# Kernel optimization log

Hardware: AMD Instinct MI355X
Metric: run time of the kernel (lower is better)

## Reference

```python
import jax, jax.numpy as jnp
import numpy as np

EMBED = 1024
B, T = 4, 2048

def setup_inputs() -> dict:
    key = jax.random.key(0)
    k1, k2, k3, k4, k5 = jax.random.split(key, 5)
    s_in = 1.0 / np.sqrt(EMBED)
    return {
        "x": jax.random.normal(k1, (B, T, EMBED), dtype=jnp.float32),
        "w_qkv": jax.random.normal(k2, (3 * EMBED, EMBED), dtype=jnp.float32) * s_in,  # torch Linear layout [out,in]
        "b_qkv": jax.random.normal(k3, (3 * EMBED,), dtype=jnp.float32) * 0.01,
        "w_proj": jax.random.normal(k4, (EMBED, EMBED), dtype=jnp.float32) * s_in,
        "b_proj": jax.random.normal(k5, (EMBED,), dtype=jnp.float32) * 0.01,
    }

def reference(x, w_qkv, b_qkv, w_proj, b_proj):
    Bq, Tq, C = x.shape
    qkv = jnp.einsum('btc,oc->bto', x, w_qkv) + b_qkv        # [B,T,3C]
    q, k, v = jnp.split(qkv, 3, axis=-1)                      # each [B,T,C]
    att = jnp.einsum('btc,bsc->bts', q, k) / jnp.sqrt(jnp.float32(C))  # [B,T,T]
    causal = jnp.tril(jnp.ones((Tq, Tq), dtype=bool))
    att = jnp.where(causal[None, :, :], att, -jnp.inf)
    att = jax.nn.softmax(att, axis=-1)
    out = jnp.einsum('bts,bsc->btc', att, v)                   # [B,T,C]
    return jnp.einsum('btc,oc->bto', out, w_proj) + b_proj
```

## Files before the change

kernel.cpp:

```cpp
#include <hip/hip_runtime.h>
#include <hip/hip_bf16.h>

typedef __hip_bfloat16 bf16;
typedef __attribute__((ext_vector_type(8))) short bf16x8;
typedef __attribute__((ext_vector_type(4))) float f32x4;

#define GLD16(gp, lp) __builtin_amdgcn_global_load_lds( \
    (const __attribute__((address_space(1))) void*)(gp), \
    (__attribute__((address_space(3))) void*)(lp), 16, 0, 0)

__global__ __launch_bounds__(256) void cvt_bf16(const float* __restrict__ in,
                                                bf16* __restrict__ out) {
    int i = (blockIdx.x * 256 + threadIdx.x) * 4;
    float4 f = *(const float4*)&in[i];
    __hip_bfloat162 p0, p1;
    p0.x = __float2bfloat16(f.x); p0.y = __float2bfloat16(f.y);
    p1.x = __float2bfloat16(f.z); p1.y = __float2bfloat16(f.w);
    *(__hip_bfloat162*)&out[i]     = p0;
    *(__hip_bfloat162*)&out[i + 2] = p1;
}

__global__ __launch_bounds__(256) void cvt_weights(
    const float* __restrict__ wq, bf16* __restrict__ wqo,
    const float* __restrict__ wp, bf16* __restrict__ wpo) {
    int blk = blockIdx.x;
    const float* in; bf16* out; int base;
    if (blk < 3072) { in = wq; out = wqo; base = blk; }
    else            { in = wp; out = wpo; base = blk - 3072; }
    int i = (base * 256 + threadIdx.x) * 4;
    float4 f = *(const float4*)&in[i];
    __hip_bfloat162 p0, p1;
    p0.x = __float2bfloat16(f.x); p0.y = __float2bfloat16(f.y);
    p1.x = __float2bfloat16(f.z); p1.y = __float2bfloat16(f.w);
    *(__hip_bfloat162*)&out[i]     = p0;
    *(__hip_bfloat162*)&out[i + 2] = p1;
}

__global__ void transpose_v(const bf16* __restrict__ V, bf16* __restrict__ Vt) {
    __shared__ bf16 tile[32][33];
    const int b = blockIdx.z;
    const int c0 = blockIdx.x * 32, t0 = blockIdx.y * 32;
    const int tx = threadIdx.x, ty = threadIdx.y;
    #pragma unroll
    for (int i = 0; i < 32; i += 8)
        tile[ty + i][tx] = V[((size_t)(b * 2048 + t0 + ty + i)) * 1024 + c0 + tx];
    __syncthreads();
    #pragma unroll
    for (int i = 0; i < 32; i += 8)
        Vt[((size_t)b * 1024 + c0 + ty + i) * 2048 + t0 + tx] = tile[tx][ty + i];
}

__global__ __launch_bounds__(256) void rowsum_p(const bf16* __restrict__ P,
                                                float* __restrict__ rs) {
    const int row = blockIdx.x;
    const int t = row & 2047;
    const int ncol = ((t >> 8) + 1) << 8;
    const bf16* prow = P + (size_t)row * 2048;
    const int tid = threadIdx.x;
    float s = 0.f;
    if (tid * 8 < ncol) {
        bf16x8 v = *(const bf16x8*)&prow[tid * 8];
        #pragma unroll
        for (int i = 0; i < 8; ++i)
            s += __bfloat162float(((const bf16*)&v)[i]);
    }
    #pragma unroll
    for (int off = 32; off; off >>= 1) s += __shfl_xor(s, off);
    __shared__ float red[4];
    const int wave = tid >> 6, lane = tid & 63;
    if (lane == 0) red[wave] = s;
    __syncthreads();
    if (tid == 0) rs[row] = red[0] + red[1] + red[2] + red[3];
}

template<int MODE>
__global__ __launch_bounds__(512, 2) void gemm256(
    const bf16* __restrict__ A, const bf16* __restrict__ B,
    const float* __restrict__ bias,
    void* __restrict__ out0, void* __restrict__ out1, void* __restrict__ out2)
{
    __shared__ bf16 As[2][256][64];
    __shared__ bf16 Bs[2][256][64];
    constexpr int LDA = (MODE == 2) ? 2048 : 1024;
    constexpr int LDB = (MODE == 2) ? 2048 : 1024;

    const int nwgx = gridDim.x;
    const int nwg = nwgx * gridDim.y;
    int wg = blockIdx.y * nwgx + blockIdx.x;
    wg = (wg & 7) * (nwg >> 3) + (wg >> 3);
    const int bx = wg % nwgx, by = wg / nwgx, bz = blockIdx.z;

    if (MODE == 1 && bx > by) return;
    const int NT = (MODE == 2) ? 4 * (by + 1) : 16;
    const int m0 = by * 256, n0 = bx * 256;

    const bf16* Ab = A;
    const bf16* Bb = B;
    if (MODE == 1) { Ab += (size_t)bz * (2048ull * 1024); Bb += (size_t)bz * (2048ull * 1024); }
    if (MODE == 2) { Ab += (size_t)bz * (2048ull * 2048); Bb += (size_t)bz * (1024ull * 2048); }

    const int tid = threadIdx.x;
    const int lane = tid & 63, wave = tid >> 6;
    const int wr = wave >> 2, wc = wave & 3;
    const int frow = lane & 15, fk = lane >> 4, fx = lane & 7;

    const int rl = tid >> 3;
    const int scol = ((tid & 7) ^ (rl & 7)) * 8;
    const bf16* pAsrc = Ab + (size_t)(m0 + rl) * LDA + scol;
    const bf16* pBsrc = Bb + (size_t)(n0 + rl) * LDB + scol;
    const int dchunk = tid * 8;

    f32x4 acc[4][4][2] = {};

    #define STG(P, LD, LDSBASE, H, K0) do { \
        GLD16((P) + (size_t)(H) * 128 * (LD) + (K0), (LDSBASE) + (H) * 8192 + dchunk); \
        GLD16((P) + (size_t)((H) * 128 + 64) * (LD) + (K0), (LDSBASE) + (H) * 8192 + 4096 + dchunk); \
    } while (0)

    {
        bf16* la = &As[0][0][0]; bf16* lb = &Bs[0][0][0];
        STG(pAsrc, LDA, la, 0, 0);
        STG(pBsrc, LDB, lb, 0, 0);
        STG(pBsrc, LDB, lb, 1, 0);
        STG(pAsrc, LDA, la, 1, 0);
        asm volatile("s_waitcnt vmcnt(4)" ::: "memory");
        __builtin_amdgcn_s_barrier();
    }

    for (int t = 0; t < NT; ++t) {
        const int buf = t & 1, nbuf = buf ^ 1;
        const int kn = (t + 1) * 64;
        bf16* lan = &As[nbuf][0][0]; bf16* lbn = &Bs[nbuf][0][0];
        const bool more = (t + 1 < NT);

        #pragma unroll
        for (int q = 0; q < 4; ++q) {
            const int aR = ((q >> 1) << 7) + wr * 64 + frow;
            const int bR = ((q & 1) << 7) + wc * 32 + frow;
            bf16x8 av[4][2], bv[2][2];
            #pragma unroll
            for (int m = 0; m < 4; ++m)
                #pragma unroll
                for (int ks = 0; ks < 2; ++ks)
                    av[m][ks] = *(const bf16x8*)
                        &As[buf][aR + m * 16][((((ks << 2) | fk) ^ fx) << 3)];
            #pragma unroll
            for (int n = 0; n < 2; ++n)
                #pragma unroll
                for (int ks = 0; ks < 2; ++ks)
                    bv[n][ks] = *(const bf16x8*)
                        &Bs[buf][bR + n * 16][((((ks << 2) | fk) ^ fx) << 3)];

            if (more) {
                if (q == 0)      STG(pAsrc, LDA, lan, 0, kn);
                else if (q == 1) STG(pBsrc, LDB, lbn, 0, kn);
                else if (q == 2) STG(pBsrc, LDB, lbn, 1, kn);
                else             STG(pAsrc, LDA, lan, 1, kn);
            }

            __builtin_amdgcn_sched_barrier(0);
            __builtin_amdgcn_s_barrier();
            asm volatile("s_waitcnt lgkmcnt(0)" ::: "memory");
            __builtin_amdgcn_sched_barrier(0);

            __builtin_amdgcn_s_setprio(1);
            #pragma unroll
            for (int m = 0; m < 4; ++m)
                #pragma unroll
                for (int n = 0; n < 2; ++n)
                    #pragma unroll
                    for (int ks = 0; ks < 2; ++ks)
                        acc[q][m][n] = __builtin_amdgcn_mfma_f32_16x16x32_bf16(
                            av[m][ks], bv[n][ks], acc[q][m][n], 0, 0, 0);
            __builtin_amdgcn_s_setprio(0);
            __builtin_amdgcn_sched_barrier(0);

            if (more) {
                if (q != 2) asm volatile("s_waitcnt vmcnt(4)" ::: "memory");
            } else {
                if (q == 0)      asm volatile("s_waitcnt vmcnt(2)" ::: "memory");
                else if (q == 1) asm volatile("s_waitcnt vmcnt(0)" ::: "memory");
            }
            __builtin_amdgcn_s_barrier();
        }
    }
    #undef STG

    #pragma unroll
    for (int q = 0; q < 4; ++q) {
        #pragma unroll
        for (int m = 0; m < 4; ++m) {
            #pragma unroll
            for (int n = 0; n < 2; ++n) {
                #pragma unroll
                for (int j = 0; j < 4; ++j) {
                    const int gr = m0 + ((q >> 1) << 7) + wr * 64 + m * 16 + (fk << 2) + j;
                    const int gc = n0 + ((q & 1) << 7) + wc * 32 + n * 16 + frow;
                    float v = acc[q][m][n][j];
                    if (MODE == 0) {
                        v += bias[gc];
                        const int which = gc >> 10;
                        const int col = gc & 1023;
                        bf16* dst = which == 0 ? (bf16*)out0
                                  : which == 1 ? (bf16*)out1 : (bf16*)out2;
                        dst[(size_t)gr * 1024 + col] = __float2bfloat16(v);
                    } else if (MODE == 1) {
                        float p = __expf(v * 0.03125f);
                        if (gc > gr) p = 0.f;
                        ((bf16*)out0)[(size_t)bz * (2048ull * 2048) +
                                      (size_t)gr * 2048 + gc] = __float2bfloat16(p);
                    } else if (MODE == 2) {
                        const float inv = 1.f / bias[bz * 2048 + gr];
                        ((bf16*)out0)[((size_t)bz * 2048 + gr) * 1024 + gc] =
                            __float2bfloat16(v * inv);
                    } else {
                        ((float*)out0)[(size_t)gr * 1024 + gc] = v + bias[gc];
                    }
                }
            }
        }
    }
}

extern "C" void kernel_launch(void* const* d_in, const int* in_sizes, int n_in,
                              void* d_out, int out_size, void* d_ws, size_t ws_size,
                              hipStream_t stream) {
    const float* x      = (const float*)d_in[0];
    const float* w_qkv  = (const float*)d_in[1];
    const float* b_qkv  = (const float*)d_in[2];
    const float* w_proj = (const float*)d_in[3];
    const float* b_proj = (const float*)d_in[4];
    float* out = (float*)d_out;
    char* ws = (char*)d_ws;

    bf16* Xb = (bf16*)(ws);
    bf16* Wq = (bf16*)(ws + 16777216);
    bf16* Wp = (bf16*)(ws + 23068672);
    bf16* Qb = (bf16*)(ws + 25165824);
    bf16* Kb = (bf16*)(ws + 41943040);
    bf16* Vb = (bf16*)(ws + 58720256);
    bf16* P  = (bf16*)(ws + 75497472);
    float* RS = (float*)(ws + 75497472 + 33554432);
    bf16* Vt = Xb;
    bf16* O  = Qb;

    hipLaunchKernelGGL(cvt_bf16, dim3(8192), dim3(256), 0, stream, x, Xb);
    hipLaunchKernelGGL(cvt_weights, dim3(4096), dim3(256), 0, stream,
                       w_qkv, Wq, w_proj, Wp);

    gemm256<0><<<dim3(12, 32, 1), 512, 0, stream>>>(
        Xb, Wq, b_qkv, (void*)Qb, (void*)Kb, (void*)Vb);

    hipLaunchKernelGGL(transpose_v, dim3(32, 64, 4), dim3(32, 8), 0, stream, Vb, Vt);

    gemm256<1><<<dim3(8, 8, 4), 512, 0, stream>>>(
        Qb, Kb, (const float*)nullptr, (void*)P, nullptr, nullptr);

    hipLaunchKernelGGL(rowsum_p, dim3(8192), dim3(256), 0, stream, P, RS);

    gemm256<2><<<dim3(4, 8, 4), 512, 0, stream>>>(
        P, Vt, (const float*)RS, (void*)O, nullptr, nullptr);

    gemm256<3><<<dim3(4, 32, 1), 512, 0, stream>>>(
        O, Wp, b_proj, (void*)out, nullptr, nullptr);
}
```

Measured before the change: 357.8 us.

## Split K for heavy causal PV row tiles and add a combine kernel

In the attention-times-V GEMM, the lower row tiles (by>=4) carry the largest causal K ranges. Each of these tiles is now split into two K halves, so they run on separate workgroups and write fp32 partials to free workspace. A new combine_pv kernel adds the two partials, applies the row-sum normalization and writes bf16. This is meant to balance work across the grid and shorten the critical path of the longest workgroups. The cost is extra fp32 partial traffic and one more launch. The workgroup-index swizzle is also removed for every GEMM mode, which may change L2 locality.

```diff
diff --git a/kernel.cpp b/kernel.cpp
--- a/kernel.cpp
+++ b/kernel.cpp
@@ -73,6 +73,26 @@
     if (tid == 0) rs[row] = red[0] + red[1] + red[2] + red[3];
 }
 
+__global__ __launch_bounds__(256) void combine_pv(const float* __restrict__ OP,
+                                                  const float* __restrict__ rs,
+                                                  bf16* __restrict__ O) {
+    int idx = (blockIdx.x * 256 + threadIdx.x) * 4;
+    const int c = idx & 1023;
+    const int rl = idx >> 10;
+    const int bz = rl >> 10, r = rl & 1023;
+    const float inv = 1.f / rs[bz * 2048 + 1024 + r];
+    const float4 a = *(const float4*)&OP[idx];
+    const float4 b = *(const float4*)&OP[4 * 1024 * 1024 + idx];
+    bf16* dst = &O[((size_t)(bz * 2048 + 1024 + r)) * 1024 + c];
+    __hip_bfloat162 p0, p1;
+    p0.x = __float2bfloat16((a.x + b.x) * inv);
+    p0.y = __float2bfloat16((a.y + b.y) * inv);
+    p1.x = __float2bfloat16((a.z + b.z) * inv);
+    p1.y = __float2bfloat16((a.w + b.w) * inv);
+    *(__hip_bfloat162*)&dst[0] = p0;
+    *(__hip_bfloat162*)&dst[2] = p1;
+}
+
 template<int MODE>
 __global__ __launch_bounds__(512, 2) void gemm256(
     const bf16* __restrict__ A, const bf16* __restrict__ B,
@@ -84,14 +104,16 @@
     constexpr int LDA = (MODE == 2) ? 2048 : 1024;
     constexpr int LDB = (MODE == 2) ? 2048 : 1024;
 
-    const int nwgx = gridDim.x;
-    const int nwg = nwgx * gridDim.y;
-    int wg = blockIdx.y * nwgx + blockIdx.x;
-    wg = (wg & 7) * (nwg >> 3) + (wg >> 3);
-    const int bx = wg % nwgx, by = wg / nwgx, bz = blockIdx.z;
-
+    const int bx = blockIdx.x, bz = blockIdx.z;
+    int by = blockIdx.y, kz = -1;
     if (MODE == 1 && bx > by) return;
+    if (MODE == 2 && by >= 4) {
+        kz = (by - 4) & 1;
+        by = 4 + ((by - 4) >> 1);
+    }
     const int NT = (MODE == 2) ? 4 * (by + 1) : 16;
+    const int t0 = (MODE == 2 && kz == 1) ? NT / 2 : 0;
+    const int t1 = (MODE == 2 && kz == 0) ? NT / 2 : NT;
     const int m0 = by * 256, n0 = bx * 256;
 
     const bf16* Ab = A;
@@ -119,19 +141,20 @@
 
     {
         bf16* la = &As[0][0][0]; bf16* lb = &Bs[0][0][0];
-        STG(pAsrc, LDA, la, 0, 0);
-        STG(pBsrc, LDB, lb, 0, 0);
-        STG(pBsrc, LDB, lb, 1, 0);
-        STG(pAsrc, LDA, la, 1, 0);
+        const int k0 = t0 * 64;
+        STG(pAsrc, LDA, la, 0, k0);
+        STG(pBsrc, LDB, lb, 0, k0);
+        STG(pBsrc, LDB, lb, 1, k0);
+        STG(pAsrc, LDA, la, 1, k0);
         asm volatile("s_waitcnt vmcnt(4)" ::: "memory");
         __builtin_amdgcn_s_barrier();
     }
 
-    for (int t = 0; t < NT; ++t) {
+    for (int t = t0; t < t1; ++t) {
         const int buf = t & 1, nbuf = buf ^ 1;
         const int kn = (t + 1) * 64;
         bf16* lan = &As[nbuf][0][0]; bf16* lbn = &Bs[nbuf][0][0];
-        const bool more = (t + 1 < NT);
+        const bool more = (t + 1 < t1);
 
         #pragma unroll
         for (int q = 0; q < 4; ++q) {
@@ -210,9 +233,15 @@
                         ((bf16*)out0)[(size_t)bz * (2048ull * 2048) +
                                       (size_t)gr * 2048 + gc] = __float2bfloat16(p);
                     } else if (MODE == 2) {
-                        const float inv = 1.f / bias[bz * 2048 + gr];
-                        ((bf16*)out0)[((size_t)bz * 2048 + gr) * 1024 + gc] =
-                            __float2bfloat16(v * inv);
+                        if (kz < 0) {
+                            const float inv = 1.f / bias[bz * 2048 + gr];
+                            ((bf16*)out0)[((size_t)bz * 2048 + gr) * 1024 + gc] =
+                                __float2bfloat16(v * inv);
+                        } else {
+                            ((float*)out1)[(size_t)kz * (4 * 1024 * 1024) +
+                                           (size_t)bz * (1024 * 1024) +
+                                           (size_t)(gr - 1024) * 1024 + gc] = v;
+                        }
                     } else {
                         ((float*)out0)[(size_t)gr * 1024 + gc] = v + bias[gc];
                     }
@@ -243,6 +272,7 @@
     float* RS = (float*)(ws + 75497472 + 33554432);
     bf16* Vt = Xb;
     bf16* O  = Qb;
+    float* OPart = (float*)(ws + 41943040);
 
     hipLaunchKernelGGL(cvt_bf16, dim3(8192), dim3(256), 0, stream, x, Xb);
     hipLaunchKernelGGL(cvt_weights, dim3(4096), dim3(256), 0, stream,
@@ -258,8 +288,11 @@
 
     hipLaunchKernelGGL(rowsum_p, dim3(8192), dim3(256), 0, stream, P, RS);
 
-    gemm256<2><<<dim3(4, 8, 4), 512, 0, stream>>>(
-        P, Vt, (const float*)RS, (void*)O, nullptr, nullptr);
+    gemm256<2><<<dim3(4, 12, 4), 512, 0, stream>>>(
+        P, Vt, (const float*)RS, (void*)O, (void*)OPart, nullptr);
+
+    hipLaunchKernelGGL(combine_pv, dim3(4096), dim3(256), 0, stream,
+                       OPart, RS, O);
 
     gemm256<3><<<dim3(4, 32, 1), 512, 0, stream>>>(
         O, Wp, b_proj, (void*)out, nullptr, nullptr);
```

Measured after the change: 356.0 us. About the same (-0.5%).
